# Kernel optimization log

Measured on AMD Instinct MI355X. Metric: run time of the kernel, lower is better.

Reference implementation:

```python
import jax, jax.numpy as jnp
import numpy as np

N = 100000   # nodes
E = 3200000  # edges (avg degree 32)
D = 128      # in_channels
H = 128      # hidden_channels
A, S, ETH = 3, 2, 3  # head output dims


def _w(k, o, i):
    return jax.random.normal(k, (o, i), dtype=jnp.float32) / np.sqrt(i).astype(np.float32)


def setup_inputs() -> dict:
    key = jax.random.key(0)
    ks = jax.random.split(key, 20)
    x = jax.random.normal(ks[0], (N, D), dtype=jnp.float32)
    edge_index = jax.random.randint(ks[1], (2, E), 0, N, dtype=jnp.int64)
    inp = {"x": x, "edge_index": edge_index}
    # SAGEConv params: Wl applied to mean-aggregated neighbors, Wr to root, plus bias
    dims = [("1", D, H), ("2", H, H), ("3", H, H), ("a", H, A), ("s", H, S), ("e", H, ETH)]
    ki = 2
    for tag, i, o in dims:
        inp[f"W{tag}l"] = _w(ks[ki], o, i); ki += 1
        inp[f"W{tag}r"] = _w(ks[ki], o, i); ki += 1
        inp[f"b{tag}"] = jnp.zeros((o,), dtype=jnp.float32)
    return inp


def _sage(x, src, dst, inv_deg, Wl, Wr, b):
    # mean aggregation of source features onto destination nodes, then linear
    agg = jax.ops.segment_sum(x[src], dst, num_segments=N) * inv_deg  # [N, d]
    return agg @ Wl.T + x @ Wr.T + b


def reference(x, edge_index,
              W1l, W1r, b1, W2l, W2r, b2, W3l, W3r, b3,
              Wal, War, ba, Wsl, Wsr, bs, Wel, Wer, be):
    src, dst = edge_index[0], edge_index[1]
    deg = jax.ops.segment_sum(jnp.ones((E,), jnp.float32), dst, num_segments=N)
    inv_deg = (1.0 / jnp.maximum(deg, 1.0))[:, None]  # [N,1]
    h = jax.nn.relu(_sage(x, src, dst, inv_deg, W1l, W1r, b1))
    h = jax.nn.relu(_sage(h, src, dst, inv_deg, W2l, W2r, b2))
    h = jax.nn.relu(_sage(h, src, dst, inv_deg, W3l, W3r, b3))
    age_out = _sage(h, src, dst, inv_deg, Wal, War, ba)
    sex_out = _sage(h, src, dst, inv_deg, Wsl, Wsr, bs)
    eth_out = _sage(h, src, dst, inv_deg, Wel, Wer, be)
    return (age_out, sex_out, eth_out)
```

## Files before the change

kernel.cpp:

```cpp
#include <hip/hip_runtime.h>

#define TPB 256
#define NB1 256
#define NBUCK 512

using half4_t = __attribute__((ext_vector_type(4))) _Float16;
using half8_t = __attribute__((ext_vector_type(8))) _Float16;
using f32x4 = __attribute__((ext_vector_type(4))) float;


__global__ __launch_bounds__(256) void histprep_k(
    const int* __restrict__ ei, int* __restrict__ hist, int E, int stripe,
    const float* __restrict__ x, _Float16* __restrict__ xh, int n4,
    const float* __restrict__ w0, const float* __restrict__ w1,
    const float* __restrict__ w2, const float* __restrict__ w3,
    const float* __restrict__ w4, const float* __restrict__ w5,
    _Float16* __restrict__ wh,
    const float* __restrict__ Wal, const float* __restrict__ War,
    const float* __restrict__ ba, const float* __restrict__ Wsl,
    const float* __restrict__ Wsr, const float* __restrict__ bsx,
    const float* __restrict__ Wel, const float* __restrict__ Wer,
    const float* __restrict__ be, _Float16* __restrict__ Wcat,
    float* __restrict__ bcat) {
  __shared__ int h[NBUCK];
  int b = blockIdx.x;
  if (b < NB1) {
    for (int i = threadIdx.x; i < NBUCK; i += 256) h[i] = 0;
    __syncthreads();
    int b0 = b * stripe;
    int b1 = min(b0 + stripe, E);
    for (int e = b0 + threadIdx.x; e < b1; e += 256) atomicAdd(&h[ei[E + e] >> 8], 1);
    __syncthreads();
    for (int i = threadIdx.x; i < NBUCK; i += 256) hist[i * NB1 + b] = h[i];
    return;
  }
  int t = (b - NB1) * TPB + threadIdx.x;
  if (t < n4) {
    float4 v = ((const float4*)x)[t];
    half4_t o;
    o.x = (_Float16)v.x; o.y = (_Float16)v.y; o.z = (_Float16)v.z; o.w = (_Float16)v.w;
    ((half4_t*)xh)[t] = o;
  }
  if (t < 6 * 4096) {
    int which = t >> 12, i = t & 4095;
    const float* src = which == 0 ? w0 : which == 1 ? w1 : which == 2 ? w2
                     : which == 3 ? w3 : which == 4 ? w4 : w5;
    float4 v = ((const float4*)src)[i];
    half4_t o;
    o.x = (_Float16)v.x; o.y = (_Float16)v.y; o.z = (_Float16)v.z; o.w = (_Float16)v.w;
    ((half4_t*)wh)[(size_t)which * 4096 + i] = o;
  }
  if (t < 2048) {
    float v = 0.f;
    if (t < 384) v = Wal[t];
    else if (t < 640) v = Wsl[t - 384];
    else if (t < 1024) v = Wel[t - 640];
    else if (t < 1408) v = War[t - 1024];
    else if (t < 1664) v = Wsr[t - 1408];
    else v = Wer[t - 1664];
    Wcat[t] = (_Float16)v;
  }
  if (t < 16) {
    float bb = 0.f;
    if (t >= 8 && t < 11) bb = ba[t - 8];
    else if (t >= 11 && t < 13) bb = bsx[t - 11];
    else if (t >= 13) bb = be[t - 13];
    bcat[t] = bb;
  }
}

__global__ void scan1_k(const int* __restrict__ src, int* __restrict__ out,
                        int* __restrict__ chunk, int n) {
  __shared__ int sh[TPB];
  int i = blockIdx.x * TPB + threadIdx.x;
  int v = (i < n) ? src[i] : 0;
  sh[threadIdx.x] = v;
  __syncthreads();
  for (int off = 1; off < TPB; off <<= 1) {
    int t = (threadIdx.x >= off) ? sh[threadIdx.x - off] : 0;
    __syncthreads();
    sh[threadIdx.x] += t;
    __syncthreads();
  }
  if (i < n) out[i] = sh[threadIdx.x] - v;
  if (threadIdx.x == TPB - 1) chunk[blockIdx.x] = sh[TPB - 1];
}

__global__ void scan2_k(int* __restrict__ chunk, int nb) {
  __shared__ int sh[512];
  int v = (threadIdx.x < nb) ? chunk[threadIdx.x] : 0;
  sh[threadIdx.x] = v;
  __syncthreads();
  for (int off = 1; off < 512; off <<= 1) {
    int t = (threadIdx.x >= off) ? sh[threadIdx.x - off] : 0;
    __syncthreads();
    sh[threadIdx.x] += t;
    __syncthreads();
  }
  if (threadIdx.x < nb) chunk[threadIdx.x] = sh[threadIdx.x] - v;
}


__global__ __launch_bounds__(256) void scatter1_k(const int* __restrict__ ei,
                                                  const int* __restrict__ base,
                                                  const int* __restrict__ chunk,
                                                  unsigned* __restrict__ ebuf, int E,
                                                  int stripe) {
  __shared__ int cur[NBUCK];
  for (int i = threadIdx.x; i < NBUCK; i += 256)
    cur[i] = base[i * NB1 + blockIdx.x] + chunk[i];
  __syncthreads();
  int b0 = blockIdx.x * stripe;
  int b1 = min(b0 + stripe, E);
  for (int e = b0 + threadIdx.x; e < b1; e += 256) {
    int s = ei[e];
    int d = ei[E + e];
    int p = atomicAdd(&cur[d >> 8], 1);
    ebuf[p] = (unsigned)s | ((unsigned)(d & 255) << 24);
  }
}

__global__ __launch_bounds__(256) void build_k(const unsigned* __restrict__ ebuf,
                                               const int* __restrict__ base,
                                               const int* __restrict__ chunk,
                                               int* __restrict__ row_start,
                                               int* __restrict__ deg,
                                               float* __restrict__ invd,
                                               int* __restrict__ csr, int N, int E) {
  __shared__ int h[256];
  __shared__ int excl[256];
  __shared__ int bse[2];
  int b = blockIdx.x;
  int t = threadIdx.x;
  if (t == 0) {
    bse[0] = base[b * NB1] + chunk[b];
    bse[1] = (b + 1 < NBUCK) ? base[(b + 1) * NB1] + chunk[b + 1] : E;
  }
  h[t] = 0;
  __syncthreads();
  int bs = bse[0], be = bse[1];
  for (int e = bs + t; e < be; e += 256) atomicAdd(&h[ebuf[e] >> 24], 1);
  __syncthreads();
  int v = h[t];
  excl[t] = v;
  __syncthreads();
  for (int off = 1; off < 256; off <<= 1) {
    int tv = (t >= off) ? excl[t - off] : 0;
    __syncthreads();
    excl[t] += tv;
    __syncthreads();
  }
  int ex = excl[t] - v;
  int node = b * 256 + t;
  if (node < N) {
    row_start[node] = bs + ex;
    deg[node] = v;
    invd[node] = 1.0f / fmaxf((float)v, 1.0f);
  }
  h[t] = bs + ex;
  __syncthreads();
  for (int e = bs + t; e < be; e += 256) {
    unsigned p = ebuf[e];
    int pos = atomicAdd(&h[p >> 24], 1);
    csr[pos] = (int)(p & 0xFFFFFFu);
  }
}


__global__ __launch_bounds__(256) void agg128_k(const _Float16* __restrict__ hb,
                                                const int* __restrict__ csr,
                                                const int* __restrict__ row_start,
                                                const int* __restrict__ deg,
                                                const float* __restrict__ invd,
                                                _Float16* __restrict__ out, int n) {
  int node = (blockIdx.x << 2) + (threadIdx.x >> 6);
  if (node >= n) return;
  int lane = threadIdx.x & 63;
  int g = lane >> 4;
  int l = lane & 15;
  int s = row_start[node];
  int c = deg[node];
  const _Float16* base = hb + (l << 3);
  float a0 = 0.f, a1 = 0.f, a2 = 0.f, a3 = 0.f;
  float a4 = 0.f, a5 = 0.f, a6 = 0.f, a7 = 0.f;
  int j = 0;
  if (c >= 16) {
    int id[4];
#pragma unroll
    for (int p = 0; p < 4; ++p) id[p] = csr[s + 4 * p + g];
    while (true) {
      half8_t v[4];
#pragma unroll
      for (int p = 0; p < 4; ++p) v[p] = *(const half8_t*)&base[(size_t)id[p] * 128];
      j += 16;
      bool more = (j + 16 <= c);
      if (more) {
#pragma unroll
        for (int p = 0; p < 4; ++p) id[p] = csr[s + j + 4 * p + g];
      }
#pragma unroll
      for (int p = 0; p < 4; ++p) {
        a0 += (float)v[p][0]; a1 += (float)v[p][1];
        a2 += (float)v[p][2]; a3 += (float)v[p][3];
        a4 += (float)v[p][4]; a5 += (float)v[p][5];
        a6 += (float)v[p][6]; a7 += (float)v[p][7];
      }
      if (!more) break;
    }
  }
  if (j < c) {
    int cm1 = c - 1;
#pragma unroll
    for (int p = 0; p < 4; ++p) {
      int e = j + 4 * p + g;
      float m = (e < c) ? 1.f : 0.f;
      int id = csr[s + min(e, cm1)];
      half8_t v = *(const half8_t*)&base[(size_t)id * 128];
      a0 = fmaf(m, (float)v[0], a0); a1 = fmaf(m, (float)v[1], a1);
      a2 = fmaf(m, (float)v[2], a2); a3 = fmaf(m, (float)v[3], a3);
      a4 = fmaf(m, (float)v[4], a4); a5 = fmaf(m, (float)v[5], a5);
      a6 = fmaf(m, (float)v[6], a6); a7 = fmaf(m, (float)v[7], a7);
    }
  }
  a0 += __shfl_xor(a0, 16); a1 += __shfl_xor(a1, 16);
  a2 += __shfl_xor(a2, 16); a3 += __shfl_xor(a3, 16);
  a4 += __shfl_xor(a4, 16); a5 += __shfl_xor(a5, 16);
  a6 += __shfl_xor(a6, 16); a7 += __shfl_xor(a7, 16);
  a0 += __shfl_xor(a0, 32); a1 += __shfl_xor(a1, 32);
  a2 += __shfl_xor(a2, 32); a3 += __shfl_xor(a3, 32);
  a4 += __shfl_xor(a4, 32); a5 += __shfl_xor(a5, 32);
  a6 += __shfl_xor(a6, 32); a7 += __shfl_xor(a7, 32);
  if (g == 0) {
    float w = invd[node];
    half8_t r;
    r[0] = (_Float16)(a0 * w); r[1] = (_Float16)(a1 * w);
    r[2] = (_Float16)(a2 * w); r[3] = (_Float16)(a3 * w);
    r[4] = (_Float16)(a4 * w); r[5] = (_Float16)(a5 * w);
    r[6] = (_Float16)(a6 * w); r[7] = (_Float16)(a7 * w);
    *(half8_t*)&out[(size_t)node * 128 + (l << 3)] = r;
  }
}


__global__ __launch_bounds__(256) void gemm2_k(
    const _Float16* __restrict__ Aagg, const _Float16* __restrict__ Ah,
    const _Float16* __restrict__ Wh,
    const float* __restrict__ bias, _Float16* __restrict__ outh,
    const _Float16* __restrict__ Wcat, const float* __restrict__ bcat,
    float* __restrict__ head_g, float* __restrict__ head_r, int n, int mode) {
  __shared__ _Float16 Ws[32768];
  int tid = threadIdx.x;
  int wave = tid >> 6;
  int lane = tid & 63;
  int g = lane >> 4;
  int l = lane & 15;
  int m0 = blockIdx.x * 64 + wave * 16;
  int arow = m0 + l;
  bool valid = arow < n;

  half8_t afA[4], afH[4];
  size_t abase = (size_t)arow * 128 + g * 8;
  if (valid) {
#pragma unroll
    for (int kb = 0; kb < 4; ++kb) afA[kb] = *(const half8_t*)&Aagg[abase + kb * 32];
#pragma unroll
    for (int kb = 0; kb < 4; ++kb) afH[kb] = *(const half8_t*)&Ah[abase + kb * 32];
  } else {
#pragma unroll
    for (int kb = 0; kb < 4; ++kb) {
#pragma unroll
      for (int jj = 0; jj < 8; ++jj) { afA[kb][jj] = (_Float16)0; afH[kb][jj] = (_Float16)0; }
    }
  }

#pragma unroll
  for (int it = 0; it < 16; ++it) {
    int ci = tid + it * 256;
    int row = ci >> 4;
    int kc = ci & 15;
    float4 v = *(const float4*)&Wh[(size_t)row * 128 + kc * 8];
    *(float4*)&Ws[(size_t)row * 128 + ((kc ^ (row & 7)) * 8)] = v;
  }
  __syncthreads();

  f32x4 acc[8];
#pragma unroll
  for (int ct = 0; ct < 8; ++ct) acc[ct] = (f32x4){0.f, 0.f, 0.f, 0.f};

#pragma unroll
  for (int kb = 0; kb < 4; ++kb) {
#pragma unroll
    for (int ct = 0; ct < 8; ++ct) {
      int row = ct * 16 + l;
      half8_t bf = *(const half8_t*)&Ws[(size_t)row * 128 + (((kb * 4 + g) ^ (l & 7)) * 8)];
      acc[ct] = __builtin_amdgcn_mfma_f32_16x16x32_f16(afA[kb], bf, acc[ct], 0, 0, 0);
    }
  }
#pragma unroll
  for (int kb = 0; kb < 4; ++kb) {
#pragma unroll
    for (int ct = 0; ct < 8; ++ct) {
      int row = 128 + ct * 16 + l;
      half8_t bf = *(const half8_t*)&Ws[(size_t)row * 128 + (((kb * 4 + g) ^ (l & 7)) * 8)];
      acc[ct] = __builtin_amdgcn_mfma_f32_16x16x32_f16(afH[kb], bf, acc[ct], 0, 0, 0);
    }
  }

  if (mode == 0) {
#pragma unroll
    for (int ct = 0; ct < 8; ++ct) {
      int col = ct * 16 + l;
      float bc = bias[col];
#pragma unroll
      for (int r = 0; r < 4; ++r) {
        int row = m0 + g * 4 + r;
        if (row < n) {
          float v = fmaxf(acc[ct][r] + bc, 0.f);
          outh[(size_t)row * 128 + col] = (_Float16)v;
        }
      }
    }
  } else {
    __syncthreads();
    _Float16* Hs = Ws + wave * 2048;
#pragma unroll
    for (int ct = 0; ct < 8; ++ct) {
      int col = ct * 16 + l;
      float bc = bias[col];
#pragma unroll
      for (int r = 0; r < 4; ++r) {
        Hs[(g * 4 + r) * 128 + col] = (_Float16)fmaxf(acc[ct][r] + bc, 0.f);
      }
    }
    f32x4 ah = (f32x4){0.f, 0.f, 0.f, 0.f};
#pragma unroll
    for (int kb = 0; kb < 4; ++kb) {
      half8_t af = *(const half8_t*)&Hs[l * 128 + kb * 32 + g * 8];
      half8_t bf = *(const half8_t*)&Wcat[(size_t)l * 128 + kb * 32 + g * 8];
      ah = __builtin_amdgcn_mfma_f32_16x16x32_f16(af, bf, ah, 0, 0, 0);
    }
    float bc = bcat[l];
#pragma unroll
    for (int r = 0; r < 4; ++r) {
      int row = m0 + g * 4 + r;
      if (row < n) {
        float v = ah[r] + bc;
        if (l < 8) head_g[(size_t)row * 8 + l] = v;
        else head_r[(size_t)row * 8 + (l - 8)] = v;
      }
    }
  }
}


__global__ void agg8_k(const float* __restrict__ head_g, const float* __restrict__ head_r,
                       const int* __restrict__ csr, const int* __restrict__ row_start,
                       const int* __restrict__ deg, const float* __restrict__ invd,
                       float* __restrict__ out, int n) {
  int node = (blockIdx.x << 2) + (threadIdx.x >> 6);
  if (node >= n) return;
  int lane = threadIdx.x & 63;
  int c2 = lane & 3;
  int g = lane >> 2;
  int s = row_start[node], cnt = deg[node];
  float ax = 0.f, ay = 0.f;
  int j = 0;
  for (; j + 32 <= cnt; j += 32) {
#pragma unroll
    for (int p = 0; p < 2; ++p) {
      int id = csr[s + j + 16 * p + g];
      float2 v = *(const float2*)&head_g[(size_t)id * 8 + 2 * c2];
      ax += v.x;
      ay += v.y;
    }
  }
  if (j < cnt) {
    int cm1 = cnt - 1;
#pragma unroll
    for (int p = 0; p < 2; ++p) {
      int e = j + 16 * p + g;
      float m = (e < cnt) ? 1.f : 0.f;
      int id = csr[s + min(e, cm1)];
      float2 v = *(const float2*)&head_g[(size_t)id * 8 + 2 * c2];
      ax = fmaf(m, v.x, ax);
      ay = fmaf(m, v.y, ay);
    }
  }
  ax += __shfl_xor(ax, 4);  ay += __shfl_xor(ay, 4);
  ax += __shfl_xor(ax, 8);  ay += __shfl_xor(ay, 8);
  ax += __shfl_xor(ax, 16); ay += __shfl_xor(ay, 16);
  ax += __shfl_xor(ax, 32); ay += __shfl_xor(ay, 32);
  if (g == 0) {
    float w = invd[node];
    float r0 = ax * w + head_r[(size_t)node * 8 + 2 * c2];
    float r1 = ay * w + head_r[(size_t)node * 8 + 2 * c2 + 1];
    float rr[2] = {r0, r1};
#pragma unroll
    for (int q = 0; q < 2; ++q) {
      int f = 2 * c2 + q;
      float r = rr[q];
      if (f < 3) out[(size_t)node * 3 + f] = r;
      else if (f < 5) out[(size_t)3 * n + (size_t)node * 2 + (f - 3)] = r;
      else out[(size_t)5 * n + (size_t)node * 3 + (f - 5)] = r;
    }
  }
}


extern "C" void kernel_launch(void* const* d_in, const int* in_sizes, int n_in,
                              void* d_out, int out_size, void* d_ws, size_t ws_size,
                              hipStream_t stream) {
  const float* x = (const float*)d_in[0];
  const int* ei = (const int*)d_in[1];
  const float* W1l = (const float*)d_in[2];
  const float* W1r = (const float*)d_in[3];
  const float* b1 = (const float*)d_in[4];
  const float* W2l = (const float*)d_in[5];
  const float* W2r = (const float*)d_in[6];
  const float* b2 = (const float*)d_in[7];
  const float* W3l = (const float*)d_in[8];
  const float* W3r = (const float*)d_in[9];
  const float* b3 = (const float*)d_in[10];
  const float* Wal = (const float*)d_in[11];
  const float* War = (const float*)d_in[12];
  const float* ba = (const float*)d_in[13];
  const float* Wsl = (const float*)d_in[14];
  const float* Wsr = (const float*)d_in[15];
  const float* bsx = (const float*)d_in[16];
  const float* Wel = (const float*)d_in[17];
  const float* Wer = (const float*)d_in[18];
  const float* be = (const float*)d_in[19];

  int N = in_sizes[0] / 128;
  int E = in_sizes[1] / 2;
  int NBKT = (N + 255) >> 8;

  char* w = (char*)d_ws;
  auto alloc = [&](size_t b) {
    char* p = w;
    w += (b + 255) & ~(size_t)255;
    return p;
  };
  int* deg = (int*)alloc((size_t)N * 4);
  int* row_start = (int*)alloc((size_t)N * 4);
  float* invd = (float*)alloc((size_t)N * 4);
  int* hist = (int*)alloc((size_t)NBUCK * NB1 * 4);
  int* chunk = (int*)alloc(512 * 4);
  int* csr = (int*)alloc((size_t)E * 4);
  unsigned* ebuf = (unsigned*)alloc((size_t)E * 4);
  _Float16* xh = (_Float16*)alloc((size_t)N * 128 * 2);
  _Float16* aggh = (_Float16*)alloc((size_t)N * 128 * 2);
  _Float16* hA = (_Float16*)alloc((size_t)N * 128 * 2);
  _Float16* hB = (_Float16*)alloc((size_t)N * 128 * 2);
  _Float16* wh = (_Float16*)alloc((size_t)6 * 16384 * 2);
  _Float16* Wcat = (_Float16*)alloc(2048 * 2);
  float* bcat = (float*)alloc(16 * 4);
  float* head_g = (float*)alloc((size_t)N * 8 * 4);
  float* head_r = (float*)alloc((size_t)N * 8 * 4);

  int stripe = (((E + NB1 - 1) / NB1) + 255) & ~255;
  int nscan = NBUCK * NB1;
  int nbScan = (nscan + TPB - 1) / TPB;
  int nbNode = (N + 3) / 4;
  int nbM = (N + 63) / 64;
  int nbC = (N * 32 + TPB - 1) / TPB;

  histprep_k<<<NB1 + nbC, TPB, 0, stream>>>(ei, hist, E, stripe, x, xh, N * 32,
                                            W1l, W1r, W2l, W2r, W3l, W3r, wh,
                                            Wal, War, ba, Wsl, Wsr, bsx, Wel, Wer,
                                            be, Wcat, bcat);
  scan1_k<<<nbScan, TPB, 0, stream>>>(hist, hist, chunk, nscan);
  scan2_k<<<1, 512, 0, stream>>>(chunk, nbScan);
  scatter1_k<<<NB1, 256, 0, stream>>>(ei, hist, chunk, ebuf, E, stripe);
  build_k<<<NBKT, 256, 0, stream>>>(ebuf, hist, chunk, row_start, deg, invd, csr, N, E);

  agg128_k<<<nbNode, TPB, 0, stream>>>(xh, csr, row_start, deg, invd, aggh, N);
  gemm2_k<<<nbM, TPB, 0, stream>>>(aggh, xh, wh + 0 * 16384, b1, hA, nullptr, nullptr,
                                   nullptr, nullptr, N, 0);
  agg128_k<<<nbNode, TPB, 0, stream>>>(hA, csr, row_start, deg, invd, aggh, N);
  gemm2_k<<<nbM, TPB, 0, stream>>>(aggh, hA, wh + 2 * 16384, b2, hB, nullptr, nullptr,
                                   nullptr, nullptr, N, 0);
  agg128_k<<<nbNode, TPB, 0, stream>>>(hB, csr, row_start, deg, invd, aggh, N);
  gemm2_k<<<nbM, TPB, 0, stream>>>(aggh, hB, wh + 4 * 16384, b3, nullptr, Wcat, bcat,
                                   head_g, head_r, N, 1);
  agg8_k<<<nbNode, TPB, 0, stream>>>(head_g, head_r, csr, row_start, deg, invd,
                                     (float*)d_out, N);
}
```

Baseline: 656.2 us.

## Stage bucket scatter through LDS and double gemm block rows

The edge scatter kernel now builds a per-block local histogram, scans it in shared memory, and scatters packed edges into an LDS staging buffer. It then writes each bucket's run to global memory contiguously, so the random scattered global writes become coalesced ones. Separately, the fused GEMM kernel is launched with 512 threads covering 128 rows per block, which halves how many times the shared weight tile is loaded. The trade-offs are a second pass over the destination indices and heavy LDS use, with the staging buffer sized to the per-block stripe (12800 entries), plus the larger GEMM blocks reduce scheduling granularity.

```diff
diff --git a/kernel.cpp b/kernel.cpp
--- a/kernel.cpp
+++ b/kernel.cpp
@@ -3,6 +3,7 @@
 #define TPB 256
 #define NB1 256
 #define NBUCK 512
+#define SBUF_CAP 12800
 
 using half4_t = __attribute__((ext_vector_type(4))) _Float16;
 using half8_t = __attribute__((ext_vector_type(8))) _Float16;
@@ -101,22 +102,53 @@
 }
 
 
+
 __global__ __launch_bounds__(256) void scatter1_k(const int* __restrict__ ei,
                                                   const int* __restrict__ base,
                                                   const int* __restrict__ chunk,
                                                   unsigned* __restrict__ ebuf, int E,
                                                   int stripe) {
-  __shared__ int cur[NBUCK];
-  for (int i = threadIdx.x; i < NBUCK; i += 256)
-    cur[i] = base[i * NB1 + blockIdx.x] + chunk[i];
-  __syncthreads();
-  int b0 = blockIdx.x * stripe;
+  __shared__ int hloc[NBUCK];
+  __shared__ int excl[NBUCK];
+  __shared__ int curs[NBUCK];
+  __shared__ int psum[256];
+  __shared__ unsigned sbuf[SBUF_CAP];
+  int t = threadIdx.x;
+  int b = blockIdx.x;
+  int b0 = b * stripe;
   int b1 = min(b0 + stripe, E);
-  for (int e = b0 + threadIdx.x; e < b1; e += 256) {
+  for (int i = t; i < NBUCK; i += 256) hloc[i] = 0;
+  __syncthreads();
+  for (int e = b0 + t; e < b1; e += 256) atomicAdd(&hloc[ei[E + e] >> 8], 1);
+  __syncthreads();
+  int c0 = hloc[2 * t], c1 = hloc[2 * t + 1];
+  psum[t] = c0 + c1;
+  __syncthreads();
+  for (int off = 1; off < 256; off <<= 1) {
+    int v = (t >= off) ? psum[t - off] : 0;
+    __syncthreads();
+    psum[t] += v;
+    __syncthreads();
+  }
+  int pe = (t > 0) ? psum[t - 1] : 0;
+  excl[2 * t] = pe;
+  excl[2 * t + 1] = pe + c0;
+  curs[2 * t] = pe;
+  curs[2 * t + 1] = pe + c0;
+  __syncthreads();
+  for (int e = b0 + t; e < b1; e += 256) {
     int s = ei[e];
     int d = ei[E + e];
-    int p = atomicAdd(&cur[d >> 8], 1);
-    ebuf[p] = (unsigned)s | ((unsigned)(d & 255) << 24);
+    int p = atomicAdd(&curs[d >> 8], 1);
+    sbuf[p] = (unsigned)s | ((unsigned)(d & 255) << 24);
+  }
+  __syncthreads();
+  int wv = t >> 6, ln = t & 63;
+  for (int i = wv; i < NBUCK; i += 4) {
+    int st = excl[i];
+    int cnt = curs[i] - st;
+    int gb = base[i * NB1 + b] + chunk[i];
+    for (int k = ln; k < cnt; k += 64) ebuf[gb + k] = sbuf[st + k];
   }
 }
 
@@ -242,7 +274,7 @@
 }
 
 
-__global__ __launch_bounds__(256) void gemm2_k(
+__global__ __launch_bounds__(512) void gemm2_k(
     const _Float16* __restrict__ Aagg, const _Float16* __restrict__ Ah,
     const _Float16* __restrict__ Wh,
     const float* __restrict__ bias, _Float16* __restrict__ outh,
@@ -254,7 +286,7 @@
   int lane = tid & 63;
   int g = lane >> 4;
   int l = lane & 15;
-  int m0 = blockIdx.x * 64 + wave * 16;
+  int m0 = blockIdx.x * 128 + wave * 16;
   int arow = m0 + l;
   bool valid = arow < n;
 
@@ -274,8 +306,8 @@
   }
 
 #pragma unroll
-  for (int it = 0; it < 16; ++it) {
-    int ci = tid + it * 256;
+  for (int it = 0; it < 8; ++it) {
+    int ci = tid + it * 512;
     int row = ci >> 4;
     int kc = ci & 15;
     float4 v = *(const float4*)&Wh[(size_t)row * 128 + kc * 8];
@@ -462,7 +494,7 @@
   int nscan = NBUCK * NB1;
   int nbScan = (nscan + TPB - 1) / TPB;
   int nbNode = (N + 3) / 4;
-  int nbM = (N + 63) / 64;
+  int nbM = (N + 127) / 128;
   int nbC = (N * 32 + TPB - 1) / TPB;
 
   histprep_k<<<NB1 + nbC, TPB, 0, stream>>>(ei, hist, E, stripe, x, xh, N * 32,
@@ -475,13 +507,13 @@
   build_k<<<NBKT, 256, 0, stream>>>(ebuf, hist, chunk, row_start, deg, invd, csr, N, E);
 
   agg128_k<<<nbNode, TPB, 0, stream>>>(xh, csr, row_start, deg, invd, aggh, N);
-  gemm2_k<<<nbM, TPB, 0, stream>>>(aggh, xh, wh + 0 * 16384, b1, hA, nullptr, nullptr,
+  gemm2_k<<<nbM, 512, 0, stream>>>(aggh, xh, wh + 0 * 16384, b1, hA, nullptr, nullptr,
                                    nullptr, nullptr, N, 0);
   agg128_k<<<nbNode, TPB, 0, stream>>>(hA, csr, row_start, deg, invd, aggh, N);
-  gemm2_k<<<nbM, TPB, 0, stream>>>(aggh, hA, wh + 2 * 16384, b2, hB, nullptr, nullptr,
+  gemm2_k<<<nbM, 512, 0, stream>>>(aggh, hA, wh + 2 * 16384, b2, hB, nullptr, nullptr,
                                    nullptr, nullptr, N, 0);
   agg128_k<<<nbNode, TPB, 0, stream>>>(hB, csr, row_start, deg, invd, aggh, N);
-  gemm2_k<<<nbM, TPB, 0, stream>>>(aggh, hB, wh + 4 * 16384, b3, nullptr, Wcat, bcat,
+  gemm2_k<<<nbM, 512, 0, stream>>>(aggh, hB, wh + 4 * 16384, b3, nullptr, Wcat, bcat,
                                    head_g, head_r, N, 1);
   agg8_k<<<nbNode, TPB, 0, stream>>>(head_g, head_r, csr, row_start, deg, invd,
                                      (float*)d_out, N);
```

Result: slower. 672.9 us (+2.5%).
